# Kernel tuning notes

Hardware: AMD Instinct MI355X
Metric: run time of the kernel (lower is better)

The kernel has to match this reference:

```python
import jax, jax.numpy as jnp
import numpy as np

K = 3        # kernel_size
STRIDE = 1
PAD = 1
DIL = 1


def setup_inputs() -> dict:
    key = jax.random.key(0)
    ks = jax.random.split(key, 5)
    B, C, H, W, O = 4, 64, 128, 128, 64
    x = jax.random.normal(ks[0], (B, C, H, W), jnp.float32)
    # small offset-conv weights -> offsets of a few pixels (realistic trained regime)
    offset_w = jax.random.normal(ks[1], (2 * K * K, C, K, K), jnp.float32) * 0.01
    offset_b = jax.random.normal(ks[2], (2 * K * K,), jnp.float32) * 0.01
    weight = jax.random.normal(ks[3], (O, C, K, K), jnp.float32)
    bias = jax.random.normal(ks[4], (O,), jnp.float32)
    return {"x": x, "offset_w": offset_w, "offset_b": offset_b,
            "weight": weight, "bias": bias}


def _conv2d(x, w, b):
    y = jax.lax.conv_general_dilated(
        x, w, window_strides=(STRIDE, STRIDE),
        padding=[(PAD, PAD), (PAD, PAD)],
        dimension_numbers=("NCHW", "OIHW", "NCHW"))
    return y + b[None, :, None, None]


def _deform_conv2d(x, offset, weight, bias):
    B, C, H, W = x.shape
    O = weight.shape[0]
    KK = K * K
    Ho, Wo = offset.shape[2], offset.shape[3]
    # offset channels ordered (y, x) per kernel tap: [B, KK, 2, Ho, Wo]
    off = offset.reshape(B, KK, 2, Ho, Wo)
    kyy, kxx = jnp.meshgrid(jnp.arange(K) * DIL, jnp.arange(K) * DIL, indexing="ij")
    kyy = kyy.reshape(KK).astype(x.dtype)
    kxx = kxx.reshape(KK).astype(x.dtype)
    base_y = (jnp.arange(Ho) * STRIDE - PAD).astype(x.dtype)
    base_x = (jnp.arange(Wo) * STRIDE - PAD).astype(x.dtype)
    # sampling positions [B, KK, Ho, Wo]
    py = base_y[None, None, :, None] + kyy[None, :, None, None] + off[:, :, 0]
    px = base_x[None, None, None, :] + kxx[None, :, None, None] + off[:, :, 1]

    y0 = jnp.floor(py); x0 = jnp.floor(px)
    y1 = y0 + 1.0;      x1 = x0 + 1.0
    wy1 = py - y0; wy0 = 1.0 - wy1
    wx1 = px - x0; wx0 = 1.0 - wx1

    xf = x.reshape(B, C, H * W)

    def corner(yc, xc):
        valid = (yc >= 0) & (yc < H) & (xc >= 0) & (xc < W)  # zero padding outside
        idx = (jnp.clip(yc, 0, H - 1) * W + jnp.clip(xc, 0, W - 1)).astype(jnp.int32)
        g = jax.vmap(lambda xb, ib: xb[:, ib.reshape(-1)])(xf, idx)  # [B, C, KK*Ho*Wo]
        g = g.reshape(B, C, KK, Ho, Wo)
        return g * valid[:, None].astype(x.dtype)

    val = (corner(y0, x0) * (wy0 * wx0)[:, None]
         + corner(y0, x1) * (wy0 * wx1)[:, None]
         + corner(y1, x0) * (wy1 * wx0)[:, None]
         + corner(y1, x1) * (wy1 * wx1)[:, None])  # [B, C, KK, Ho, Wo]

    out = jnp.einsum("bckhw,ock->bohw", val, weight.reshape(O, C, KK))
    return out + bias[None, :, None, None]


def reference(x, offset_w, offset_b, weight, bias):
    offset = _conv2d(x, offset_w, offset_b)
    return _deform_conv2d(x, offset, weight, bias)
```

## Files before the change

### kernel.cpp

```cpp
#include <hip/hip_runtime.h>

#define B_   4
#define C_   64
#define O_   64
#define H_   128
#define W_   128
#define HW_  (H_ * W_)
#define KK_  9
#define M_   18

typedef short  short8  __attribute__((ext_vector_type(8)));
typedef float  floatx4 __attribute__((ext_vector_type(4)));
typedef float  float2v __attribute__((ext_vector_type(2)));
typedef unsigned int   uint4v   __attribute__((ext_vector_type(4)));
typedef unsigned short ushort4v __attribute__((ext_vector_type(4)));
typedef unsigned short ushort8v __attribute__((ext_vector_type(8)));

static __device__ __forceinline__ unsigned short f2bf(float f) {
    unsigned int u = __float_as_uint(f);
    u += 0x7FFFu + ((u >> 16) & 1u);
    return (unsigned short)(u >> 16);
}
static __device__ __forceinline__ float bf2f(unsigned short s) {
    return __uint_as_float((unsigned int)s << 16);
}
static __device__ __forceinline__ float2v bf2x(unsigned int q) {
    float2v r;
    r.x = __uint_as_float(q << 16);
    r.y = __uint_as_float(q & 0xFFFF0000u);
    return r;
}

__global__ __launch_bounds__(256) void prep(
        const float* __restrict__ x, const float* __restrict__ w,
        const float* __restrict__ ow, unsigned short* __restrict__ xT,
        unsigned short* __restrict__ wtbf, unsigned short* __restrict__ owtbf) {
    const int blk = blockIdx.x;
    if (blk < 1024) {
        __shared__ unsigned short T[64][72];
        const int tid  = threadIdx.x;
        const int half = blk & 1;
        const int y    = (blk >> 1) & (H_ - 1);
        const int b    = blk >> 8;
        const float* xby = x + (size_t)b * C_ * HW_ + y * W_ + half * 64;
        for (int i = tid; i < C_ * 64; i += 256) {
            const int c = i >> 6, xc = i & 63;
            T[xc][c] = f2bf(xby[(size_t)c * HW_ + xc]);
        }
        __syncthreads();
        unsigned short* dst = xT + (size_t)b * (4 * HW_ * 16) + y * (W_ * 16)
                                 + half * (64 * 16);
        for (int j = tid; j < 1024; j += 256) {
            const int g  = j >> 8;
            const int x8 = (j >> 2) & 63;
            const int c0 = (j & 3) * 4;
            const ushort4v pk = *(const ushort4v*)&T[x8][g * 16 + c0];
            *(ushort4v*)&dst[(size_t)g * (HW_ * 16) + x8 * 16 + c0] = pk;
        }
    } else if (blk < 1042) {
        const int i = (blk - 1024) * 256 + threadIdx.x;
        const int lane = i & 63, rest = i >> 6;
        const int ot = rest & 3, cks = rest >> 2;
        const int chunk = cks / 6, ks = cks % 6;
        const int o = ot * 16 + (lane & 15);
        const int kbase = chunk * 192 + ks * 32 + (lane >> 4) * 8;
        ushort8v pk;
        #pragma unroll
        for (int j = 0; j < 8; ++j) {
            const int k = kbase + j;
            pk[j] = f2bf(w[o * 576 + (k & 63) * 9 + (k >> 6)]);
        }
        *(ushort8v*)&wtbf[(size_t)i * 8] = pk;
    } else {
        const int i = (blk - 1042) * 256 + threadIdx.x;
        const int lane = i & 63, rest = i >> 6;
        const int tile = rest & 1, tks = rest >> 1;
        const int tap = tks >> 1, ks = tks & 1;
        const int m = tile * 16 + (lane & 15);
        const int cb = ks * 32 + (lane >> 4) * 8;
        ushort8v pk;
        #pragma unroll
        for (int j = 0; j < 8; ++j)
            pk[j] = (m < M_) ? f2bf(ow[m * 576 + (cb + j) * 9 + tap])
                             : (unsigned short)0;
        *(ushort8v*)&owtbf[(size_t)i * 8] = pk;
    }
}

__global__ __launch_bounds__(256, 4) void dcn_fused(
        const unsigned short* __restrict__ xT,
        const unsigned short* __restrict__ owtbf, const float* __restrict__ ob,
        const unsigned short* __restrict__ wtbf, const float* __restrict__ bias,
        float* __restrict__ out) {
    __shared__ union {
        unsigned short P[3][66][72];
        float ep[4][64][17];
    } u;
    __shared__ float offs[4][M_][16];

    const int tid    = threadIdx.x;
    const int lane   = tid & 63;
    const int wslot  = __builtin_amdgcn_readfirstlane(tid >> 6);
    const int lane15 = lane & 15;
    const int quad   = lane >> 4;

    const int g    = blockIdx.x;
    const int xcd  = g & 7;
    const int slot = g >> 3;
    const int ho   = xcd * 16 + (slot >> 3);
    const int b    = (slot >> 1) & 3;
    const int wo_base = (slot & 1) << 6;

    const unsigned short* xTb = xT + (size_t)b * (4 * HW_ * 16);

    #pragma unroll
    for (int it = 0; it < 3; ++it) {
        const int t  = it * 4 + wslot;
        const int ky = t >> 2, cgp = t & 3;
        const int y  = ho - 1 + ky;
        const bool yv = (unsigned)y < (unsigned)H_;
        const unsigned short* src = xTb + (size_t)cgp * (HW_ * 16) + y * (W_ * 16);
        #pragma unroll
        for (int pass = 0; pass < 2; ++pass) {
            const int r = pass * 64 + lane;
            if (r < 66) {
                const int cx = wo_base + r - 1;
                ushort8v p0 = {0, 0, 0, 0, 0, 0, 0, 0};
                ushort8v p1 = {0, 0, 0, 0, 0, 0, 0, 0};
                if (yv && (unsigned)cx < (unsigned)W_) {
                    p0 = *(const ushort8v*)&src[cx * 16];
                    p1 = *(const ushort8v*)&src[cx * 16 + 8];
                }
                *(ushort8v*)&u.P[ky][r][cgp * 16]     = p0;
                *(ushort8v*)&u.P[ky][r][cgp * 16 + 8] = p1;
            }
        }
    }
    __syncthreads();

    floatx4 oa0 = (floatx4){0.f, 0.f, 0.f, 0.f};
    floatx4 oa1 = (floatx4){0.f, 0.f, 0.f, 0.f};
    {
        const int pxt = wslot;
        #pragma unroll
        for (int ky = 0; ky < 3; ++ky) {
            #pragma unroll
            for (int kx = 0; kx < 3; ++kx) {
                const int tap = ky * 3 + kx;
                #pragma unroll
                for (int ks = 0; ks < 2; ++ks) {
                    const int kk = ks * 32 + quad * 8;
                    const short8 af =
                        *(const short8*)&u.P[ky][pxt * 16 + lane15 + kx][kk];
                    const int fb = ((tap * 2 + ks) * 2) * 64 + lane;
                    const short8 bf0 = *(const short8*)&owtbf[(size_t)fb * 8];
                    const short8 bf1 =
                        *(const short8*)&owtbf[(size_t)(fb + 64) * 8];
                    oa0 = __builtin_amdgcn_mfma_f32_16x16x32_bf16(af, bf0, oa0, 0, 0, 0);
                    oa1 = __builtin_amdgcn_mfma_f32_16x16x32_bf16(af, bf1, oa1, 0, 0, 0);
                }
            }
        }
    }
    {
        const float ob0 = ob[lane15];
        #pragma unroll
        for (int r = 0; r < 4; ++r) oa0[r] += ob0;
        *(floatx4*)&offs[wslot][lane15][quad * 4] = oa0;
        if (lane15 < 2) {
            const float ob1 = ob[16 + lane15];
            #pragma unroll
            for (int r = 0; r < 4; ++r) oa1[r] += ob1;
            *(floatx4*)&offs[wslot][16 + lane15][quad * 4] = oa1;
        }
    }
    __syncthreads();

    const int p   = wslot;
    const int pxg = p * 16 + lane15;
    floatx4 acc[4];
    #pragma unroll
    for (int t = 0; t < 4; ++t) acc[t] = (floatx4){0.f, 0.f, 0.f, 0.f};

    for (int chunk = 0; chunk < 3; ++chunk) {
        #pragma unroll
        for (int tl = 0; tl < 3; ++tl) {
            const int k  = chunk * 3 + tl;
            const int ky = k / 3, kx = k % 3;
            const float offy = offs[wslot][2 * k][lane15];
            const float offx = offs[wslot][2 * k + 1][lane15];
            const float py  = (float)(ho - 1 + ky) + offy;
            const float pxx = (float)(wo_base - 1 + kx + pxg) + offx;
            const float fy = floorf(py), fx = floorf(pxx);
            const int y0 = (int)fy, x0 = (int)fx;
            const int y1 = y0 + 1,  x1 = x0 + 1;
            const float wy1 = py - fy,  wy0 = 1.f - wy1;
            const float wx1 = pxx - fx, wx0 = 1.f - wx1;
            const bool y0v = (unsigned)y0 < (unsigned)H_;
            const bool y1v = (unsigned)y1 < (unsigned)H_;
            const bool x0v = (unsigned)x0 < (unsigned)W_;
            const bool x1v = (unsigned)x1 < (unsigned)W_;
            const float w00 = (y0v && x0v) ? wy0 * wx0 : 0.f;
            const float w01 = (y0v && x1v) ? wy0 * wx1 : 0.f;
            const float w10 = (y1v && x0v) ? wy1 * wx0 : 0.f;
            const float w11 = (y1v && x1v) ? wy1 * wx1 : 0.f;
            const float2v w00_2 = {w00, w00};
            const float2v w01_2 = {w01, w01};
            const float2v w10_2 = {w10, w10};
            const float2v w11_2 = {w11, w11};
            const int ry0 = min(max(y0, 0), H_ - 1);
            const int ry1 = min(max(y1, 0), H_ - 1);
            const int cx0 = min(max(x0, 0), W_ - 1);
            const int cx1 = min(max(x1, 0), W_ - 1);
            const int a00 = (ry0 * W_ + cx0) * 16;
            const int a01 = (ry0 * W_ + cx1) * 16;
            const int a10 = (ry1 * W_ + cx0) * 16;
            const int a11 = (ry1 * W_ + cx1) * 16;
            #pragma unroll
            for (int chalf = 0; chalf < 2; ++chalf) {
                const int c0 = chalf * 32 + quad * 8;
                const unsigned short* xp =
                    xTb + (size_t)(c0 >> 4) * (HW_ * 16) + (c0 & 8);
                const uint4v q00 = *(const uint4v*)&xp[a00];
                const uint4v q01 = *(const uint4v*)&xp[a01];
                const uint4v q10 = *(const uint4v*)&xp[a10];
                const uint4v q11 = *(const uint4v*)&xp[a11];
                uint4v pw;
                #pragma unroll
                for (int j = 0; j < 4; ++j) {
                    float2v v = bf2x(q00[j]) * w00_2;
                    v = bf2x(q01[j]) * w01_2 + v;
                    v = bf2x(q10[j]) * w10_2 + v;
                    v = bf2x(q11[j]) * w11_2 + v;
                    pw[j] = __builtin_amdgcn_perm(
                        __float_as_uint(v.y) + 0x8000u,
                        __float_as_uint(v.x) + 0x8000u,
                        0x07060302u);
                }
                const short8 af = *(const short8*)&pw;
                const int cks = chunk * 6 + tl * 2 + chalf;
                #pragma unroll
                for (int t = 0; t < 4; ++t) {
                    const short8 bfrag = *(const short8*)
                        &wtbf[(size_t)((cks * 4 + t) * 64 + lane) * 8];
                    acc[t] = __builtin_amdgcn_mfma_f32_16x16x32_bf16(
                                 af, bfrag, acc[t], 0, 0, 0);
                }
            }
        }
    }

    float* epw = &u.ep[wslot][0][0];
    #pragma unroll
    for (int t = 0; t < 4; ++t)
        #pragma unroll
        for (int r = 0; r < 4; ++r)
            epw[(t * 16 + lane15) * 17 + quad * 4 + r] = acc[t][r];

    const int wo = wo_base + p * 16 + lane15;
    #pragma unroll
    for (int i = 0; i < 16; ++i) {
        const int o = i * 4 + quad;
        out[(size_t)(b * O_ + o) * HW_ + ho * W_ + wo] =
            epw[o * 17 + lane15] + bias[o];
    }
}

extern "C" void kernel_launch(void* const* d_in, const int* in_sizes, int n_in,
                              void* d_out, int out_size, void* d_ws, size_t ws_size,
                              hipStream_t stream) {
    const float* x    = (const float*)d_in[0];
    const float* ow   = (const float*)d_in[1];
    const float* ob   = (const float*)d_in[2];
    const float* w    = (const float*)d_in[3];
    const float* bias = (const float*)d_in[4];
    float* out = (float*)d_out;

    unsigned short* wtbf  = (unsigned short*)d_ws;
    unsigned short* owtbf = wtbf + 4608 * 8;
    unsigned short* xT    = owtbf + 2304 * 8;

    prep<<<1051, 256, 0, stream>>>(x, w, ow, xT, wtbf, owtbf);
    dcn_fused<<<B_ * H_ * (W_ / 64), 256, 0, stream>>>(xT, owtbf, ob, wtbf, bias, out);
}
```

Baseline: 111.9 us.

## Switch xT to pixel-major 64-channel layout and use packed FMA in bilinear gather

The bf16 transposed input changes from four 16-channel group planes to a single NHWC-style layout holding all 64 channels contiguously per pixel. Each bilinear corner then reads its channels from one contiguous 128-byte line instead of four separate planes, which improves cache-line use in the random gather. The interpolation arithmetic uses explicit v_pk_mul/v_pk_fma inline asm, and the tap loop is flattened to a non-unrolled 9-iteration loop. That loop form lowers code size and register pressure, at the cost of less cross-tap scheduling freedom.

```diff
diff --git a/kernel.cpp b/kernel.cpp
--- a/kernel.cpp
+++ b/kernel.cpp
@@ -13,22 +13,28 @@
 typedef float  floatx4 __attribute__((ext_vector_type(4)));
 typedef float  float2v __attribute__((ext_vector_type(2)));
 typedef unsigned int   uint4v   __attribute__((ext_vector_type(4)));
-typedef unsigned short ushort4v __attribute__((ext_vector_type(4)));
 typedef unsigned short ushort8v __attribute__((ext_vector_type(8)));
 
 static __device__ __forceinline__ unsigned short f2bf(float f) {
     unsigned int u = __float_as_uint(f);
     u += 0x7FFFu + ((u >> 16) & 1u);
     return (unsigned short)(u >> 16);
-}
-static __device__ __forceinline__ float bf2f(unsigned short s) {
-    return __uint_as_float((unsigned int)s << 16);
 }
 static __device__ __forceinline__ float2v bf2x(unsigned int q) {
     float2v r;
     r.x = __uint_as_float(q << 16);
     r.y = __uint_as_float(q & 0xFFFF0000u);
     return r;
+}
+static __device__ __forceinline__ float2v pk_mul(float2v a, float2v b) {
+    float2v d;
+    asm("v_pk_mul_f32 %0, %1, %2" : "=v"(d) : "v"(a), "v"(b));
+    return d;
+}
+static __device__ __forceinline__ float2v pk_fma(float2v a, float2v b, float2v c) {
+    float2v d;
+    asm("v_pk_fma_f32 %0, %1, %2, %3" : "=v"(d) : "v"(a), "v"(b), "v"(c));
+    return d;
 }
 
 __global__ __launch_bounds__(256) void prep(
@@ -43,19 +49,16 @@
         const int y    = (blk >> 1) & (H_ - 1);
         const int b    = blk >> 8;
         const float* xby = x + (size_t)b * C_ * HW_ + y * W_ + half * 64;
-        for (int i = tid; i < C_ * 64; i += 256) {
+        for (int i = tid; i < 64 * 64; i += 256) {
             const int c = i >> 6, xc = i & 63;
             T[xc][c] = f2bf(xby[(size_t)c * HW_ + xc]);
         }
         __syncthreads();
-        unsigned short* dst = xT + (size_t)b * (4 * HW_ * 16) + y * (W_ * 16)
-                                 + half * (64 * 16);
-        for (int j = tid; j < 1024; j += 256) {
-            const int g  = j >> 8;
-            const int x8 = (j >> 2) & 63;
-            const int c0 = (j & 3) * 4;
-            const ushort4v pk = *(const ushort4v*)&T[x8][g * 16 + c0];
-            *(ushort4v*)&dst[(size_t)g * (HW_ * 16) + x8 * 16 + c0] = pk;
+        unsigned short* dst = xT + ((size_t)b * HW_ + y * W_ + half * 64) * 64;
+        for (int j = tid; j < 512; j += 256) {
+            const int x8 = j >> 3, c8 = j & 7;
+            const ushort8v pk = *(const ushort8v*)&T[x8][c8 * 8];
+            *(ushort8v*)&dst[x8 * 64 + c8 * 8] = pk;
         }
     } else if (blk < 1042) {
         const int i = (blk - 1024) * 256 + threadIdx.x;
@@ -111,29 +114,20 @@
     const int b    = (slot >> 1) & 3;
     const int wo_base = (slot & 1) << 6;
 
-    const unsigned short* xTb = xT + (size_t)b * (4 * HW_ * 16);
-
-    #pragma unroll
-    for (int it = 0; it < 3; ++it) {
-        const int t  = it * 4 + wslot;
-        const int ky = t >> 2, cgp = t & 3;
+    const unsigned short* xTb = xT + (size_t)b * HW_ * 64;
+
+    #pragma unroll
+    for (int ky = 0; ky < 3; ++ky) {
         const int y  = ho - 1 + ky;
         const bool yv = (unsigned)y < (unsigned)H_;
-        const unsigned short* src = xTb + (size_t)cgp * (HW_ * 16) + y * (W_ * 16);
-        #pragma unroll
-        for (int pass = 0; pass < 2; ++pass) {
-            const int r = pass * 64 + lane;
-            if (r < 66) {
-                const int cx = wo_base + r - 1;
-                ushort8v p0 = {0, 0, 0, 0, 0, 0, 0, 0};
-                ushort8v p1 = {0, 0, 0, 0, 0, 0, 0, 0};
-                if (yv && (unsigned)cx < (unsigned)W_) {
-                    p0 = *(const ushort8v*)&src[cx * 16];
-                    p1 = *(const ushort8v*)&src[cx * 16 + 8];
-                }
-                *(ushort8v*)&u.P[ky][r][cgp * 16]     = p0;
-                *(ushort8v*)&u.P[ky][r][cgp * 16 + 8] = p1;
-            }
+        const unsigned short* src = xTb + (size_t)y * W_ * 64;
+        for (int j = tid; j < 66 * 8; j += 256) {
+            const int r = j >> 3, c8 = j & 7;
+            const int cx = wo_base + r - 1;
+            ushort8v p0 = {0, 0, 0, 0, 0, 0, 0, 0};
+            if (yv && (unsigned)cx < (unsigned)W_)
+                p0 = *(const ushort8v*)&src[cx * 64 + c8 * 8];
+            *(ushort8v*)&u.P[ky][r][c8 * 8] = p0;
         }
     }
     __syncthreads();
@@ -176,76 +170,70 @@
     }
     __syncthreads();
 
-    const int p   = wslot;
-    const int pxg = p * 16 + lane15;
+    const int pxg = wslot * 16 + lane15;
     floatx4 acc[4];
     #pragma unroll
     for (int t = 0; t < 4; ++t) acc[t] = (floatx4){0.f, 0.f, 0.f, 0.f};
 
-    for (int chunk = 0; chunk < 3; ++chunk) {
-        #pragma unroll
-        for (int tl = 0; tl < 3; ++tl) {
-            const int k  = chunk * 3 + tl;
-            const int ky = k / 3, kx = k % 3;
-            const float offy = offs[wslot][2 * k][lane15];
-            const float offx = offs[wslot][2 * k + 1][lane15];
-            const float py  = (float)(ho - 1 + ky) + offy;
-            const float pxx = (float)(wo_base - 1 + kx + pxg) + offx;
-            const float fy = floorf(py), fx = floorf(pxx);
-            const int y0 = (int)fy, x0 = (int)fx;
-            const int y1 = y0 + 1,  x1 = x0 + 1;
-            const float wy1 = py - fy,  wy0 = 1.f - wy1;
-            const float wx1 = pxx - fx, wx0 = 1.f - wx1;
-            const bool y0v = (unsigned)y0 < (unsigned)H_;
-            const bool y1v = (unsigned)y1 < (unsigned)H_;
-            const bool x0v = (unsigned)x0 < (unsigned)W_;
-            const bool x1v = (unsigned)x1 < (unsigned)W_;
-            const float w00 = (y0v && x0v) ? wy0 * wx0 : 0.f;
-            const float w01 = (y0v && x1v) ? wy0 * wx1 : 0.f;
-            const float w10 = (y1v && x0v) ? wy1 * wx0 : 0.f;
-            const float w11 = (y1v && x1v) ? wy1 * wx1 : 0.f;
-            const float2v w00_2 = {w00, w00};
-            const float2v w01_2 = {w01, w01};
-            const float2v w10_2 = {w10, w10};
-            const float2v w11_2 = {w11, w11};
-            const int ry0 = min(max(y0, 0), H_ - 1);
-            const int ry1 = min(max(y1, 0), H_ - 1);
-            const int cx0 = min(max(x0, 0), W_ - 1);
-            const int cx1 = min(max(x1, 0), W_ - 1);
-            const int a00 = (ry0 * W_ + cx0) * 16;
-            const int a01 = (ry0 * W_ + cx1) * 16;
-            const int a10 = (ry1 * W_ + cx0) * 16;
-            const int a11 = (ry1 * W_ + cx1) * 16;
-            #pragma unroll
-            for (int chalf = 0; chalf < 2; ++chalf) {
-                const int c0 = chalf * 32 + quad * 8;
-                const unsigned short* xp =
-                    xTb + (size_t)(c0 >> 4) * (HW_ * 16) + (c0 & 8);
-                const uint4v q00 = *(const uint4v*)&xp[a00];
-                const uint4v q01 = *(const uint4v*)&xp[a01];
-                const uint4v q10 = *(const uint4v*)&xp[a10];
-                const uint4v q11 = *(const uint4v*)&xp[a11];
-                uint4v pw;
-                #pragma unroll
-                for (int j = 0; j < 4; ++j) {
-                    float2v v = bf2x(q00[j]) * w00_2;
-                    v = bf2x(q01[j]) * w01_2 + v;
-                    v = bf2x(q10[j]) * w10_2 + v;
-                    v = bf2x(q11[j]) * w11_2 + v;
-                    pw[j] = __builtin_amdgcn_perm(
-                        __float_as_uint(v.y) + 0x8000u,
-                        __float_as_uint(v.x) + 0x8000u,
-                        0x07060302u);
-                }
-                const short8 af = *(const short8*)&pw;
-                const int cks = chunk * 6 + tl * 2 + chalf;
-                #pragma unroll
-                for (int t = 0; t < 4; ++t) {
-                    const short8 bfrag = *(const short8*)
-                        &wtbf[(size_t)((cks * 4 + t) * 64 + lane) * 8];
-                    acc[t] = __builtin_amdgcn_mfma_f32_16x16x32_bf16(
-                                 af, bfrag, acc[t], 0, 0, 0);
-                }
+    #pragma unroll 1
+    for (int k = 0; k < 9; ++k) {
+        const int ky = k / 3, kx = k - ky * 3;
+        const float offy = offs[wslot][2 * k][lane15];
+        const float offx = offs[wslot][2 * k + 1][lane15];
+        const float py  = (float)(ho - 1 + ky) + offy;
+        const float pxx = (float)(wo_base - 1 + kx + pxg) + offx;
+        const float fy = floorf(py), fx = floorf(pxx);
+        const int y0 = (int)fy, x0 = (int)fx;
+        const int y1 = y0 + 1,  x1 = x0 + 1;
+        const float wy1 = py - fy,  wy0 = 1.f - wy1;
+        const float wx1 = pxx - fx, wx0 = 1.f - wx1;
+        const bool y0v = (unsigned)y0 < (unsigned)H_;
+        const bool y1v = (unsigned)y1 < (unsigned)H_;
+        const bool x0v = (unsigned)x0 < (unsigned)W_;
+        const bool x1v = (unsigned)x1 < (unsigned)W_;
+        const float w00 = (y0v && x0v) ? wy0 * wx0 : 0.f;
+        const float w01 = (y0v && x1v) ? wy0 * wx1 : 0.f;
+        const float w10 = (y1v && x0v) ? wy1 * wx0 : 0.f;
+        const float w11 = (y1v && x1v) ? wy1 * wx1 : 0.f;
+        const float2v w00_2 = {w00, w00};
+        const float2v w01_2 = {w01, w01};
+        const float2v w10_2 = {w10, w10};
+        const float2v w11_2 = {w11, w11};
+        const int ry0 = min(max(y0, 0), H_ - 1);
+        const int ry1 = min(max(y1, 0), H_ - 1);
+        const int cx0 = min(max(x0, 0), W_ - 1);
+        const int cx1 = min(max(x1, 0), W_ - 1);
+        const int a00 = (ry0 * W_ + cx0) * 64;
+        const int a01 = (ry0 * W_ + cx1) * 64;
+        const int a10 = (ry1 * W_ + cx0) * 64;
+        const int a11 = (ry1 * W_ + cx1) * 64;
+        #pragma unroll
+        for (int chalf = 0; chalf < 2; ++chalf) {
+            const unsigned short* xp = xTb + chalf * 32 + quad * 8;
+            const uint4v q00 = *(const uint4v*)&xp[a00];
+            const uint4v q01 = *(const uint4v*)&xp[a01];
+            const uint4v q10 = *(const uint4v*)&xp[a10];
+            const uint4v q11 = *(const uint4v*)&xp[a11];
+            uint4v pw;
+            #pragma unroll
+            for (int j = 0; j < 4; ++j) {
+                float2v v = pk_mul(bf2x(q00[j]), w00_2);
+                v = pk_fma(bf2x(q01[j]), w01_2, v);
+                v = pk_fma(bf2x(q10[j]), w10_2, v);
+                v = pk_fma(bf2x(q11[j]), w11_2, v);
+                pw[j] = __builtin_amdgcn_perm(
+                    __float_as_uint(v.y) + 0x8000u,
+                    __float_as_uint(v.x) + 0x8000u,
+                    0x07060302u);
+            }
+            const short8 af = *(const short8*)&pw;
+            const int cks = k * 2 + chalf;
+            const unsigned short* wb = wtbf + (size_t)cks * 2048 + lane * 8;
+            #pragma unroll
+            for (int t = 0; t < 4; ++t) {
+                const short8 bfrag = *(const short8*)&wb[(size_t)t * 512];
+                acc[t] = __builtin_amdgcn_mfma_f32_16x16x32_bf16(
+                             af, bfrag, acc[t], 0, 0, 0);
             }
         }
     }
@@ -257,7 +245,7 @@
         for (int r = 0; r < 4; ++r)
             epw[(t * 16 + lane15) * 17 + quad * 4 + r] = acc[t][r];
 
-    const int wo = wo_base + p * 16 + lane15;
+    const int wo = wo_base + wslot * 16 + lane15;
     #pragma unroll
     for (int i = 0; i < 16; ++i) {
         const int o = i * 4 + quad;
```

Result: slower. 125.5 us (+12.2%).
